# Optimization experiments

Hardware: AMD Instinct MI355X
Metric: run time of the kernel (lower is better)

## Reference

```python
import jax, jax.numpy as jnp
import numpy as np
import math

BL, N, T, C, H = 16, 256, 32, 256, 4
HD = C // H
GEOM_DIM = 12
K_REL = 32
LN_EPS = 1e-5
GEPS = 1e-6
NEG = -1e9


def setup_inputs() -> dict:
    key = jax.random.key(0)
    ks = jax.random.split(key, 24)
    s = 0.02  # weight init scale
    d = {
        "x": jax.random.normal(ks[0], (BL, N, C), jnp.float32),
        "lang_fea": jax.random.normal(ks[1], (BL, T, C), jnp.float32),
        "centers": jax.random.normal(ks[2], (BL, N, 3), jnp.float32),
        "corners": jax.random.normal(ks[3], (BL, N, 8, 3), jnp.float32),
        "obj_mask": jnp.ones((BL, N), dtype=bool),
        # LayerNorm
        "ln_g": jnp.ones((C,), jnp.float32),
        "ln_b": jnp.zeros((C,), jnp.float32),
        # qkv / proj
        "W_qkv": s * jax.random.normal(ks[4], (C, 3 * C), jnp.float32),
        "b_qkv": jnp.zeros((3 * C,), jnp.float32),
        "W_proj": s * jax.random.normal(ks[5], (C, C), jnp.float32),
        "b_proj": jnp.zeros((C,), jnp.float32),
        # geom2bias MLP (12 -> C -> H)
        "Wg1": s * jax.random.normal(ks[6], (GEOM_DIM, C), jnp.float32),
        "bg1": jnp.zeros((C,), jnp.float32),
        "Wg2": s * jax.random.normal(ks[7], (C, H), jnp.float32),
        "bg2": jnp.zeros((H,), jnp.float32),
        # txt2head MLP (C -> C -> H)
        "Wt1": s * jax.random.normal(ks[8], (C, C), jnp.float32),
        "bt1": jnp.zeros((C,), jnp.float32),
        "Wt2": s * jax.random.normal(ks[9], (C, H), jnp.float32),
        "bt2": jnp.zeros((H,), jnp.float32),
        "alpha": jnp.float32(0.05),
    }
    return d


def _build_relation_geom(centers, corners):
    # centers: (BL,N,3), corners: (BL,N,8,3) -> (BL,N,N,12)
    rel_vec = centers[:, None, :, :] - centers[:, :, None, :]  # (BL,N,N,3) j - i
    dist = jnp.linalg.norm(rel_vec, axis=-1, keepdims=True)
    horiz_dist = jnp.linalg.norm(rel_vec[..., :2], axis=-1, keepdims=True)
    delta_z = rel_vec[..., 2:3]
    cos_elev = delta_z / (dist + GEPS)
    sizes = corners.max(axis=2) - corners.min(axis=2)  # (BL,N,3)
    size_i = sizes[:, :, None, :]
    size_j = sizes[:, None, :, :]
    size_diff = size_j - size_i
    size_ratio = size_j / (size_i + GEPS)
    return jnp.concatenate([rel_vec, dist, horiz_dist, cos_elev, size_diff, size_ratio], axis=-1)


def _knn_mask(centers, k):
    # (BL,N,N) bool: each row i keeps its k nearest columns j (incl. self)
    diff = centers[:, :, None, :] - centers[:, None, :, :]
    dist = jnp.linalg.norm(diff, axis=-1)  # (BL,N,N)
    _, idx = jax.lax.top_k(-dist, k)  # smallest-k indices, (BL,N,k)
    return jnp.any(jax.nn.one_hot(idx, dist.shape[-1], dtype=bool), axis=-2)


def reference(x, lang_fea, centers, corners, obj_mask, ln_g, ln_b,
              W_qkv, b_qkv, W_proj, b_proj, Wg1, bg1, Wg2, bg2,
              Wt1, bt1, Wt2, bt2, alpha):
    # geometric pairwise bias: (BL,N,N,12) -> MLP -> (BL,H,N,N)
    geom = _build_relation_geom(centers, corners)
    bias = jax.nn.gelu(geom @ Wg1 + bg1, approximate=False) @ Wg2 + bg2
    bias = jnp.transpose(bias, (0, 3, 1, 2))  # (BL,H,N,N)

    # language-conditioned head gate: (BL,H,1,1)
    sent = lang_fea.mean(axis=1)  # (BL,C)
    head_w = jax.nn.sigmoid(jax.nn.gelu(sent @ Wt1 + bt1, approximate=False) @ Wt2 + bt2)
    head_w = head_w[:, :, None, None]

    warm = 1.0  # epoch=None -> no warmup scaling

    knn_mask = _knn_mask(centers, K_REL)
    pair = obj_mask[:, :, None] & obj_mask[:, None, :]
    attn_mask = knn_mask & pair  # (BL,N,N)

    residual = x
    # LayerNorm
    mu = x.mean(axis=-1, keepdims=True)
    var = x.var(axis=-1, keepdims=True)
    xn = (x - mu) * jax.lax.rsqrt(var + LN_EPS) * ln_g + ln_b

    qkv = (xn @ W_qkv + b_qkv).reshape(BL, N, 3, H, HD)
    q = jnp.transpose(qkv[:, :, 0], (0, 2, 1, 3))  # (BL,H,N,HD)
    k = jnp.transpose(qkv[:, :, 1], (0, 2, 1, 3))
    v = jnp.transpose(qkv[:, :, 2], (0, 2, 1, 3))

    logits = jnp.einsum("bhid,bhjd->bhij", q, k) / math.sqrt(HD)
    bias_eff = warm * alpha * head_w * bias
    logits = logits + bias_eff
    logits = jnp.where(attn_mask[:, None, :, :], logits, NEG)

    attn = jax.nn.softmax(logits, axis=-1)  # dropout is identity at eval
    out = jnp.einsum("bhij,bhjd->bhid", attn, v)
    out = jnp.transpose(out, (0, 2, 1, 3)).reshape(BL, N, C)
    out = out @ W_proj + b_proj
    x_out = residual + out
    return (x_out, jax.lax.stop_gradient(attn), jax.lax.stop_gradient(bias_eff))
```

## Files before the change

### kernel.cpp

```cpp
#include <hip/hip_runtime.h>
#include <math.h>

#define BLn 16
#define Nn 256
#define Tn 32
#define Cn 256
#define Hn 4
#define HDn 64
#define KREL 32

typedef float f32x4 __attribute__((ext_vector_type(4)));
typedef __bf16 bf16x8 __attribute__((ext_vector_type(8)));

#define MFMA16(a, b, c) __builtin_amdgcn_mfma_f32_16x16x32_bf16(a, b, c, 0, 0, 0)

union frag_u {
    bf16x8 v;
    uint2 u[2];
};

__device__ __forceinline__ float gelu_exact(float x) {
    return 0.5f * x * (1.0f + erff(x * 0.70710678118654752440f));
}

__device__ __forceinline__ float gelu_sig(float x) {
    float e = __builtin_amdgcn_exp2f(-2.4554669f * x);
    return x * __builtin_amdgcn_rcpf(1.0f + e);
}

__global__ void __launch_bounds__(256) k_prep(
    const float* __restrict__ x, const float* __restrict__ ln_g, const float* __restrict__ ln_b,
    __bf16* __restrict__ xnb, const float* __restrict__ centers, const int* __restrict__ obj,
    unsigned char* __restrict__ knn, const float* __restrict__ corners,
    float* __restrict__ sizes, const float* __restrict__ lang, const float* __restrict__ Wt1,
    const float* __restrict__ bt1, const float* __restrict__ Wt2, const float* __restrict__ bt2,
    float* __restrict__ headw, const float* __restrict__ W_qkv, __bf16* __restrict__ wqT,
    const float* __restrict__ W_proj, __bf16* __restrict__ wpT) {
    __shared__ float4 d4[64];
    __shared__ float sm1[Nn];
    __shared__ float ss[4], qq[4];
    __shared__ float T[64][65];
    float* sm0 = (float*)d4;
    int blk = blockIdx.x;
    int tid = threadIdx.x;

    if (blk < 4096) {
        int row = blk;
        int c = tid;
        float v = x[(size_t)row * Cn + c];
        float s = v, q = v * v;
        for (int m = 32; m > 0; m >>= 1) {
            s += __shfl_xor(s, m, 64);
            q += __shfl_xor(q, m, 64);
        }
        int w = c >> 6, l = c & 63;
        if (l == 0) { ss[w] = s; qq[w] = q; }
        __syncthreads();
        s = ss[0] + ss[1] + ss[2] + ss[3];
        q = qq[0] + qq[1] + qq[2] + qq[3];
        float mu = s * (1.0f / Cn);
        float var = q * (1.0f / Cn) - mu * mu;
        float r = rsqrtf(var + 1e-5f);
        xnb[(size_t)row * Cn + c] = (__bf16)((v - mu) * r * ln_g[c] + ln_b[c]);
    } else if (blk < 8192) {
        int bi = blk - 4096;
        int b = bi >> 8, i = bi & 255;
        int j = tid;
        float cx = centers[(b * Nn + i) * 3 + 0];
        float cy = centers[(b * Nn + i) * 3 + 1];
        float cz = centers[(b * Nn + i) * 3 + 2];
        float dx = centers[(b * Nn + j) * 3 + 0] - cx;
        float dy = centers[(b * Nn + j) * 3 + 1] - cy;
        float dz = centers[(b * Nn + j) * 3 + 2] - cz;
        float dd = sqrtf(dx * dx + dy * dy + dz * dz);
        sm0[j] = dd;
        __syncthreads();
        int rank = 0;
        for (int t4 = 0; t4 < 64; t4++) {
            float4 o = d4[t4];
            int t = t4 * 4;
            rank += (o.x < dd) || (o.x == dd && t + 0 < j);
            rank += (o.y < dd) || (o.y == dd && t + 1 < j);
            rank += (o.z < dd) || (o.z == dd && t + 2 < j);
            rank += (o.w < dd) || (o.w == dd && t + 3 < j);
        }
        bool m = (rank < KREL);
        m = m && (obj[b * Nn + i] != 0) && (obj[b * Nn + j] != 0);
        knn[(size_t)bi * Nn + j] = m ? 1 : 0;
    } else if (blk < 8208) {
        int b = blk - 8192, n = tid;
        const float* p = corners + (size_t)((b * Nn + n) * 8) * 3;
        float mn[3] = {1e30f, 1e30f, 1e30f}, mx[3] = {-1e30f, -1e30f, -1e30f};
        for (int v = 0; v < 8; v++)
            for (int d = 0; d < 3; d++) {
                float t = p[v * 3 + d];
                mn[d] = fminf(mn[d], t);
                mx[d] = fmaxf(mx[d], t);
            }
        for (int d = 0; d < 3; d++) sizes[(b * Nn + n) * 3 + d] = mx[d] - mn[d];
    } else if (blk < 8224) {
        int b = blk - 8208, c = tid;
        float s = 0.0f;
        for (int t = 0; t < Tn; t++) s += lang[((size_t)b * Tn + t) * Cn + c];
        sm0[c] = s * (1.0f / Tn);
        __syncthreads();
        float acc = bt1[c];
        for (int i = 0; i < Cn; i++) acc += sm0[i] * Wt1[i * Cn + c];
        sm1[c] = gelu_exact(acc);
        __syncthreads();
        if (c < Hn) {
            float a = bt2[c];
            for (int i = 0; i < Cn; i++) a += sm1[i] * Wt2[i * Hn + c];
            headw[b * Hn + c] = 1.0f / (1.0f + expf(-a));
        }
    } else if (blk < 8272) {
        int t = blk - 8224;
        int kt = t & 3, ot = t >> 2;
        for (int itr = 0; itr < 16; itr++) {
            int idx = itr * 256 + tid;
            int r = idx >> 6, c = idx & 63;
            T[r][c] = W_qkv[(size_t)(kt * 64 + r) * 768 + ot * 64 + c];
        }
        __syncthreads();
        for (int itr = 0; itr < 16; itr++) {
            int idx = itr * 256 + tid;
            int r = idx >> 6, c = idx & 63;
            wqT[(size_t)(ot * 64 + r) * 256 + kt * 64 + c] = (__bf16)T[c][r];
        }
    } else {
        int t = blk - 8272;
        int kt = t & 3, ot = t >> 2;
        for (int itr = 0; itr < 16; itr++) {
            int idx = itr * 256 + tid;
            int r = idx >> 6, c = idx & 63;
            T[r][c] = W_proj[(size_t)(kt * 64 + r) * 256 + ot * 64 + c];
        }
        __syncthreads();
        for (int itr = 0; itr < 16; itr++) {
            int idx = itr * 256 + tid;
            int r = idx >> 6, c = idx & 63;
            wpT[(size_t)(ot * 64 + r) * 256 + kt * 64 + c] = (__bf16)T[c][r];
        }
    }
}

__global__ void __launch_bounds__(256, 5) k_heavy(
    const float* __restrict__ centers, const float* __restrict__ sizes,
    const float* __restrict__ Wg1, const float* __restrict__ bg1,
    const float* __restrict__ Wg2, const float* __restrict__ bg2,
    const float* __restrict__ headw, const float* __restrict__ alphap,
    float* __restrict__ bias_eff, const __bf16* __restrict__ xnb,
    const __bf16* __restrict__ wqT, const float* __restrict__ bqkv,
    __bf16* __restrict__ qkvb) {
    __shared__ __bf16 fT[Nn][16];
    __shared__ __bf16 W1T[257][20];
    __shared__ __bf16 W2T[4][260];
    __shared__ __bf16 gbuf[4][32][40];

    int blk = blockIdx.x;
    int tid = threadIdx.x;

    if (blk >= 4096) {
        int t = blk - 4096;
        int ib = t & 63, y = t >> 6;
        int w = tid >> 6, l = tid & 63, lr = l & 15, lg = l >> 4;
        const __bf16* arow = xnb + (size_t)(ib * 64 + w * 16 + lr) * Cn;

        f32x4 acc[4];
#pragma unroll
        for (int ot = 0; ot < 4; ot++) acc[ot] = (f32x4){0.f, 0.f, 0.f, 0.f};
#pragma unroll
        for (int kc = 0; kc < 8; kc++) {
            bf16x8 af = *(const bf16x8*)(arow + kc * 32 + lg * 8);
#pragma unroll
            for (int ot = 0; ot < 4; ot++) {
                bf16x8 bfr = *(const bf16x8*)(wqT + (size_t)(y * 64 + ot * 16 + lr) * Cn +
                                              kc * 32 + lg * 8);
                acc[ot] = MFMA16(af, bfr, acc[ot]);
            }
        }
        int seg = y >> 2, h = y & 3;
        __bf16* segp = qkvb + (size_t)seg * 1048576;
#pragma unroll
        for (int ot = 0; ot < 4; ot++) {
            float bo = bqkv[y * 64 + ot * 16 + lr];
#pragma unroll
            for (int r = 0; r < 4; r++) {
                int ig = ib * 64 + w * 16 + lg * 4 + r;
                int b = ig >> 8, n = ig & 255;
                segp[(((size_t)(b * Hn + h)) * Nn + n) * HDn + ot * 16 + lr] =
                    (__bf16)(acc[ot][r] + bo);
            }
        }
        return;
    }

    int b = blk >> 8, i = blk & 255;

    {
        int c = tid;
        __bf16 t1[20];
#pragma unroll
        for (int k = 0; k < 12; k++) t1[k] = (__bf16)Wg1[k * Cn + c];
        t1[12] = (__bf16)bg1[c];
#pragma unroll
        for (int k = 13; k < 20; k++) t1[k] = (__bf16)0.f;
#pragma unroll
        for (int q = 0; q < 5; q++) *(uint2*)&W1T[c][q * 4] = *(uint2*)&t1[q * 4];
#pragma unroll
        for (int h = 0; h < Hn; h++) W2T[h][c] = (__bf16)Wg2[c * Hn + h];
    }
    {
        int j = tid;
        float ci0 = centers[(b * Nn + i) * 3 + 0];
        float ci1 = centers[(b * Nn + i) * 3 + 1];
        float ci2 = centers[(b * Nn + i) * 3 + 2];
        float si0 = sizes[(b * Nn + i) * 3 + 0];
        float si1 = sizes[(b * Nn + i) * 3 + 1];
        float si2 = sizes[(b * Nn + i) * 3 + 2];
        float cj0 = centers[(b * Nn + j) * 3 + 0];
        float cj1 = centers[(b * Nn + j) * 3 + 1];
        float cj2 = centers[(b * Nn + j) * 3 + 2];
        float sj0 = sizes[(b * Nn + j) * 3 + 0];
        float sj1 = sizes[(b * Nn + j) * 3 + 1];
        float sj2 = sizes[(b * Nn + j) * 3 + 2];
        float rx = cj0 - ci0, ry = cj1 - ci1, rz = cj2 - ci2;
        float h2 = rx * rx + ry * ry;
        float dist = sqrtf(h2 + rz * rz);
        float horiz = sqrtf(h2);
        float f[16];
        f[0] = rx; f[1] = ry; f[2] = rz;
        f[3] = dist; f[4] = horiz;
        f[5] = rz / (dist + 1e-6f);
        f[6] = sj0 - si0; f[7] = sj1 - si1; f[8] = sj2 - si2;
        f[9] = sj0 / (si0 + 1e-6f);
        f[10] = sj1 / (si1 + 1e-6f);
        f[11] = sj2 / (si2 + 1e-6f);
        f[12] = 1.0f;
        __bf16 tf[16];
#pragma unroll
        for (int k = 0; k < 13; k++) tf[k] = (__bf16)f[k];
#pragma unroll
        for (int k = 13; k < 16; k++) tf[k] = (__bf16)0.f;
        *(bf16x8*)&fT[j][0] = *(bf16x8*)&tf[0];
        *(bf16x8*)&fT[j][8] = *(bf16x8*)&tf[8];
    }
    __syncthreads();

    int w = tid >> 6, l = tid & 63;
    int lr = l & 15, lg = l >> 4;
    int jw = w * 64;
    int lgc = (lg < 2) ? lg : 1;
    bool hk = (lg < 2);
    int lrc = (lr < 4) ? lr : 3;
    bool hr = (lr < 4);

    bf16x8 zf;
#pragma unroll
    for (int e = 0; e < 8; e++) zf[e] = (__bf16)0.f;
    f32x4 zero4 = {0.f, 0.f, 0.f, 0.f};

    bf16x8 bf_[4];
#pragma unroll
    for (int jt = 0; jt < 4; jt++) {
        bf16x8 v = *(const bf16x8*)&fT[jw + jt * 16 + lr][lgc * 8];
        bf_[jt] = hk ? v : zf;
    }

    f32x4 pacc[4];
#pragma unroll
    for (int jt = 0; jt < 4; jt++) pacc[jt] = zero4;

    for (int cc = 0; cc < 8; cc++) {
        int cbase = cc * 32;
        bf16x8 aw[2];
#pragma unroll
        for (int ct = 0; ct < 2; ct++) {
            frag_u fu;
            const __bf16* p = &W1T[cbase + ct * 16 + lr][lgc * 8];
            fu.u[0] = *(const uint2*)p;
            fu.u[1] = *(const uint2*)(p + 4);
            aw[ct] = hk ? fu.v : zf;
        }
        frag_u f2;
        {
            const __bf16* p2 = &W2T[lrc][cbase + lg * 8];
            f2.u[0] = *(const uint2*)p2;
            f2.u[1] = *(const uint2*)(p2 + 4);
        }
        bf16x8 b2 = hr ? f2.v : zf;

#pragma unroll
        for (int jp = 0; jp < 2; jp++) {
#pragma unroll
            for (int j2 = 0; j2 < 2; j2++) {
                int jt = jp * 2 + j2;
                f32x4 a0 = MFMA16(aw[0], bf_[jt], zero4);
                f32x4 a1 = MFMA16(aw[1], bf_[jt], zero4);
                __bf16 g0[4], g1[4];
#pragma unroll
                for (int r = 0; r < 4; r++) {
                    g0[r] = (__bf16)gelu_sig(a0[r]);
                    g1[r] = (__bf16)gelu_sig(a1[r]);
                }
                *(uint2*)&gbuf[w][j2 * 16 + lr][lg * 4] = *(uint2*)g0;
                *(uint2*)&gbuf[w][j2 * 16 + lr][16 + lg * 4] = *(uint2*)g1;
            }
#pragma unroll
            for (int j2 = 0; j2 < 2; j2++) {
                int jt = jp * 2 + j2;
                bf16x8 a2 = *(const bf16x8*)&gbuf[w][j2 * 16 + lr][lg * 8];
                pacc[jt] = MFMA16(a2, b2, pacc[jt]);
            }
        }
    }

    float alpha = alphap[0];
    if (hr) {
        float hw_ = headw[b * Hn + lr];
        float bg = bg2[lr];
        float* dst = bias_eff + (((size_t)(b * Hn + lr)) * Nn + i) * Nn;
#pragma unroll
        for (int jt = 0; jt < 4; jt++) {
            f32x4 o4;
#pragma unroll
            for (int r = 0; r < 4; r++) o4[r] = alpha * hw_ * (pacc[jt][r] + bg);
            *(f32x4*)&dst[jw + jt * 16 + lg * 4] = o4;
        }
    }
}

__global__ void __launch_bounds__(256) k_attn(const __bf16* __restrict__ qkvb,
                                              const float* __restrict__ bias_eff,
                                              const unsigned char* __restrict__ knn,
                                              float* __restrict__ attn_out,
                                              __bf16* __restrict__ houtb) {
    __shared__ __bf16 Vt[64][264];
    __shared__ __bf16 Plds[4][16][136];
    int blk = blockIdx.x;
    int bh = blk >> 2, it = blk & 3;
    int b = bh >> 2, h = bh & 3;
    int tid = threadIdx.x;

    const __bf16* vbase = qkvb + 2 * 1048576 + (size_t)bh * (Nn * HDn);
    {
        int j = tid;
#pragma unroll
        for (int c8 = 0; c8 < 8; c8++) {
            bf16x8 v8 = *(const bf16x8*)(vbase + (size_t)j * HDn + c8 * 8);
#pragma unroll
            for (int e = 0; e < 8; e++) Vt[c8 * 8 + e][j] = v8[e];
        }
    }
    __syncthreads();

    int w = tid >> 6, l = tid & 63;
    int lr = l & 15, lg = l >> 4;
    int i_glob = it * 64 + w * 16 + lr;

    const __bf16* qrow = qkvb + (size_t)bh * (Nn * HDn) + (size_t)i_glob * HDn;
    bf16x8 qf0 = *(const bf16x8*)(qrow + lg * 8);
    bf16x8 qf1 = *(const bf16x8*)(qrow + 32 + lg * 8);

    const __bf16* kbase = qkvb + 1048576 + (size_t)bh * (Nn * HDn);
    f32x4 s[16];
#pragma unroll
    for (int jt = 0; jt < 16; jt++) {
        const __bf16* krow = kbase + (size_t)(jt * 16 + lr) * HDn;
        bf16x8 ka = *(const bf16x8*)(krow + lg * 8);
        bf16x8 kb = *(const bf16x8*)(krow + 32 + lg * 8);
        f32x4 acc = (f32x4){0.f, 0.f, 0.f, 0.f};
        acc = MFMA16(ka, qf0, acc);
        acc = MFMA16(kb, qf1, acc);
        s[jt] = acc;
    }

    const float* brow = bias_eff + ((size_t)bh * Nn + i_glob) * Nn;
    const unsigned int* mrow = (const unsigned int*)(knn + ((size_t)(b * Nn + i_glob)) * Nn);
    float mx = -1e30f;
#pragma unroll
    for (int jt = 0; jt < 16; jt++) {
        f32x4 bi = *(const f32x4*)(brow + jt * 16 + lg * 4);
        unsigned int mk = mrow[jt * 4 + lg];
#pragma unroll
        for (int r = 0; r < 4; r++) {
            float v = fmaf(s[jt][r], 0.125f, bi[r]);
            v = ((mk >> (8 * r)) & 0xff) ? v : -1e9f;
            s[jt][r] = v;
            mx = fmaxf(mx, v);
        }
    }
    mx = fmaxf(mx, __shfl_xor(mx, 16, 64));
    mx = fmaxf(mx, __shfl_xor(mx, 32, 64));
    float sum = 0.0f;
#pragma unroll
    for (int jt = 0; jt < 16; jt++)
#pragma unroll
        for (int r = 0; r < 4; r++) {
            float e = __builtin_amdgcn_exp2f((s[jt][r] - mx) * 1.44269504f);
            s[jt][r] = e;
            sum += e;
        }
    sum += __shfl_xor(sum, 16, 64);
    sum += __shfl_xor(sum, 32, 64);
    float inv = 1.0f / sum;

    float* arow = attn_out + ((size_t)bh * Nn + i_glob) * Nn;
#pragma unroll
    for (int jt = 0; jt < 16; jt++) {
        f32x4 o4;
#pragma unroll
        for (int r = 0; r < 4; r++) {
            float a = s[jt][r] * inv;
            s[jt][r] = a;
            o4[r] = a;
        }
        *(f32x4*)(arow + jt * 16 + lg * 4) = o4;
    }

    f32x4 o[4];
#pragma unroll
    for (int dt = 0; dt < 4; dt++) o[dt] = (f32x4){0.f, 0.f, 0.f, 0.f};
    for (int half = 0; half < 2; half++) {
#pragma unroll
        for (int jr = 0; jr < 8; jr++) {
            int jt = half * 8 + jr;
            __bf16 pb[4];
#pragma unroll
            for (int r = 0; r < 4; r++) pb[r] = (__bf16)s[jt][r];
            *(uint2*)&Plds[w][lr][jr * 16 + lg * 4] = *(uint2*)pb;
        }
#pragma unroll
        for (int kk = 0; kk < 4; kk++) {
            bf16x8 pfrag = *(const bf16x8*)&Plds[w][lr][kk * 32 + lg * 8];
#pragma unroll
            for (int dt = 0; dt < 4; dt++) {
                bf16x8 vfrag = *(const bf16x8*)&Vt[dt * 16 + lr][half * 128 + kk * 32 + lg * 8];
                o[dt] = MFMA16(vfrag, pfrag, o[dt]);
            }
        }
    }

    __bf16* hrow = houtb + ((size_t)(b * Nn + i_glob)) * Cn + h * HDn;
#pragma unroll
    for (int dt = 0; dt < 4; dt++) {
        __bf16 hb[4];
#pragma unroll
        for (int r = 0; r < 4; r++) hb[r] = (__bf16)o[dt][r];
        *(uint2*)(hrow + dt * 16 + lg * 4) = *(uint2*)hb;
    }
}

__global__ void __launch_bounds__(256) k_proj(const __bf16* __restrict__ houtb,
                                              const __bf16* __restrict__ wpT,
                                              const float* __restrict__ bp,
                                              const float* __restrict__ x,
                                              float* __restrict__ xout) {
    int ib = blockIdx.x, y = blockIdx.y;
    int tid = threadIdx.x;
    int w = tid >> 6, l = tid & 63, lr = l & 15, lg = l >> 4;
    const __bf16* arow = houtb + (size_t)(ib * 64 + w * 16 + lr) * Cn;

    f32x4 acc[4];
#pragma unroll
    for (int ot = 0; ot < 4; ot++) acc[ot] = (f32x4){0.f, 0.f, 0.f, 0.f};
#pragma unroll
    for (int kc = 0; kc < 8; kc++) {
        bf16x8 af = *(const bf16x8*)(arow + kc * 32 + lg * 8);
#pragma unroll
        for (int ot = 0; ot < 4; ot++) {
            bf16x8 bfr = *(const bf16x8*)(wpT + (size_t)(y * 64 + ot * 16 + lr) * Cn +
                                          kc * 32 + lg * 8);
            acc[ot] = MFMA16(af, bfr, acc[ot]);
        }
    }
#pragma unroll
    for (int ot = 0; ot < 4; ot++) {
        int o = y * 64 + ot * 16 + lr;
        float bo = bp[o];
#pragma unroll
        for (int r = 0; r < 4; r++) {
            int ig = ib * 64 + w * 16 + lg * 4 + r;
            size_t idx = (size_t)ig * Cn + o;
            xout[idx] = x[idx] + bo + acc[ot][r];
        }
    }
}

extern "C" void kernel_launch(void* const* d_in, const int* in_sizes, int n_in,
                              void* d_out, int out_size, void* d_ws, size_t ws_size,
                              hipStream_t stream) {
    const float* x       = (const float*)d_in[0];
    const float* lang    = (const float*)d_in[1];
    const float* centers = (const float*)d_in[2];
    const float* corners = (const float*)d_in[3];
    const int*   obj     = (const int*)d_in[4];
    const float* ln_g    = (const float*)d_in[5];
    const float* ln_b    = (const float*)d_in[6];
    const float* W_qkv   = (const float*)d_in[7];
    const float* b_qkv   = (const float*)d_in[8];
    const float* W_proj  = (const float*)d_in[9];
    const float* b_proj  = (const float*)d_in[10];
    const float* Wg1     = (const float*)d_in[11];
    const float* bg1     = (const float*)d_in[12];
    const float* Wg2     = (const float*)d_in[13];
    const float* bg2     = (const float*)d_in[14];
    const float* Wt1     = (const float*)d_in[15];
    const float* bt1     = (const float*)d_in[16];
    const float* Wt2     = (const float*)d_in[17];
    const float* bt2     = (const float*)d_in[18];
    const float* alpha   = (const float*)d_in[19];

    float* out = (float*)d_out;
    float* xout     = out;
    float* attn     = out + 1048576;
    float* bias_eff = out + 5242880;

    __bf16* xnb   = (__bf16*)d_ws;
    __bf16* qkvb  = xnb + 1048576;
    __bf16* houtb = qkvb + 3145728;
    __bf16* wqT   = houtb + 1048576;
    __bf16* wpT   = wqT + 196608;
    float*  sizes = (float*)(wpT + 65536);
    float*  headw = sizes + 12288;
    unsigned char* knn = (unsigned char*)(headw + 64);

    k_prep<<<8288, 256, 0, stream>>>(x, ln_g, ln_b, xnb, centers, obj, knn, corners, sizes,
                                     lang, Wt1, bt1, Wt2, bt2, headw, W_qkv, wqT, W_proj, wpT);
    k_heavy<<<4864, 256, 0, stream>>>(centers, sizes, Wg1, bg1, Wg2, bg2, headw, alpha,
                                      bias_eff, xnb, wqT, b_qkv, qkvb);
    k_attn<<<256, 256, 0, stream>>>(qkvb, bias_eff, knn, attn, houtb);
    k_proj<<<dim3(64, 4), 256, 0, stream>>>(houtb, wpT, b_proj, x, xout);
}
```

Measured before the change: 144.8 us.

## Use fp16 16x16x16 MFMA with packed polynomial GELU in geometry-bias MLP

Replaces the bf16 32-K MFMA geom-bias MLP with fp16 16x16x16 MFMAs. The GELU output stays in registers and feeds the second MFMA directly, which removes the LDS round trip through gbuf. GELU becomes a packed fp16 clamped polynomial instead of exp2/rcp, and wasted padded K lanes are no longer computed. Risks include fp16 accuracy of the approximate GELU and lower occupancy from the launch bound changing from 5 to 4.

Result: faster. 122.0 us (-15.7%).

```diff
diff --git a/kernel.cpp b/kernel.cpp
--- a/kernel.cpp
+++ b/kernel.cpp
@@ -11,21 +11,35 @@
 
 typedef float f32x4 __attribute__((ext_vector_type(4)));
 typedef __bf16 bf16x8 __attribute__((ext_vector_type(8)));
+typedef _Float16 f16x4 __attribute__((ext_vector_type(4)));
+typedef _Float16 f16x2 __attribute__((ext_vector_type(2)));
 
 #define MFMA16(a, b, c) __builtin_amdgcn_mfma_f32_16x16x32_bf16(a, b, c, 0, 0, 0)
-
-union frag_u {
-    bf16x8 v;
-    uint2 u[2];
-};
+#define MFMA16H(a, b, c) __builtin_amdgcn_mfma_f32_16x16x16f16(a, b, c, 0, 0, 0)
 
 __device__ __forceinline__ float gelu_exact(float x) {
     return 0.5f * x * (1.0f + erff(x * 0.70710678118654752440f));
 }
 
-__device__ __forceinline__ float gelu_sig(float x) {
-    float e = __builtin_amdgcn_exp2f(-2.4554669f * x);
-    return x * __builtin_amdgcn_rcpf(1.0f + e);
+__device__ __forceinline__ f16x2 gelu_pk(f16x2 x) {
+    const f16x2 P4 = {(_Float16)4.0f, (_Float16)4.0f};
+    const f16x2 M4 = {(_Float16)-4.0f, (_Float16)-4.0f};
+    const f16x2 C0 = {(_Float16)0.833076f, (_Float16)0.833076f};
+    const f16x2 C1 = {(_Float16)-0.139388f, (_Float16)-0.139388f};
+    const f16x2 C2 = {(_Float16)0.013040f, (_Float16)0.013040f};
+    const f16x2 C3 = {(_Float16)-0.000413f, (_Float16)-0.000413f};
+    const f16x2 HF = {(_Float16)0.5f, (_Float16)0.5f};
+    const f16x2 ONE = {(_Float16)1.0f, (_Float16)1.0f};
+    const f16x2 ZERO = {(_Float16)0.0f, (_Float16)0.0f};
+    f16x2 xc = __builtin_elementwise_min(__builtin_elementwise_max(x, M4), P4);
+    f16x2 v = xc * xc;
+    f16x2 w = C3 * v + C2;
+    w = w * v + C1;
+    w = w * v + C0;
+    f16x2 t = w * xc;
+    f16x2 s = t * HF + HF;
+    s = __builtin_elementwise_min(__builtin_elementwise_max(s, ZERO), ONE);
+    return x * s;
 }
 
 __global__ void __launch_bounds__(256) k_prep(
@@ -144,7 +158,7 @@
     }
 }
 
-__global__ void __launch_bounds__(256, 5) k_heavy(
+__global__ void __launch_bounds__(256, 4) k_heavy(
     const float* __restrict__ centers, const float* __restrict__ sizes,
     const float* __restrict__ Wg1, const float* __restrict__ bg1,
     const float* __restrict__ Wg2, const float* __restrict__ bg2,
@@ -152,10 +166,9 @@
     float* __restrict__ bias_eff, const __bf16* __restrict__ xnb,
     const __bf16* __restrict__ wqT, const float* __restrict__ bqkv,
     __bf16* __restrict__ qkvb) {
-    __shared__ __bf16 fT[Nn][16];
-    __shared__ __bf16 W1T[257][20];
-    __shared__ __bf16 W2T[4][260];
-    __shared__ __bf16 gbuf[4][32][40];
+    __shared__ __align__(16) _Float16 fT[Nn][20];
+    __shared__ __align__(16) _Float16 W1T[Cn][20];
+    __shared__ __align__(16) _Float16 W2T[16][264];
 
     int blk = blockIdx.x;
     int tid = threadIdx.x;
@@ -199,16 +212,17 @@
 
     {
         int c = tid;
-        __bf16 t1[20];
-#pragma unroll
-        for (int k = 0; k < 12; k++) t1[k] = (__bf16)Wg1[k * Cn + c];
-        t1[12] = (__bf16)bg1[c];
-#pragma unroll
-        for (int k = 13; k < 20; k++) t1[k] = (__bf16)0.f;
+        _Float16 t1[20];
+#pragma unroll
+        for (int k = 0; k < 12; k++) t1[k] = (_Float16)Wg1[k * Cn + c];
+        t1[12] = (_Float16)bg1[c];
+#pragma unroll
+        for (int k = 13; k < 20; k++) t1[k] = (_Float16)0.f;
 #pragma unroll
         for (int q = 0; q < 5; q++) *(uint2*)&W1T[c][q * 4] = *(uint2*)&t1[q * 4];
 #pragma unroll
-        for (int h = 0; h < Hn; h++) W2T[h][c] = (__bf16)Wg2[c * Hn + h];
+        for (int h = 0; h < 16; h++)
+            W2T[h][c] = (h < Hn) ? (_Float16)Wg2[c * Hn + h] : (_Float16)0.f;
     }
     {
         int j = tid;
@@ -237,86 +251,50 @@
         f[10] = sj1 / (si1 + 1e-6f);
         f[11] = sj2 / (si2 + 1e-6f);
         f[12] = 1.0f;
-        __bf16 tf[16];
-#pragma unroll
-        for (int k = 0; k < 13; k++) tf[k] = (__bf16)f[k];
-#pragma unroll
-        for (int k = 13; k < 16; k++) tf[k] = (__bf16)0.f;
-        *(bf16x8*)&fT[j][0] = *(bf16x8*)&tf[0];
-        *(bf16x8*)&fT[j][8] = *(bf16x8*)&tf[8];
+        _Float16 tf[20];
+#pragma unroll
+        for (int k = 0; k < 13; k++) tf[k] = (_Float16)f[k];
+#pragma unroll
+        for (int k = 13; k < 20; k++) tf[k] = (_Float16)0.f;
+#pragma unroll
+        for (int q = 0; q < 5; q++) *(uint2*)&fT[j][q * 4] = *(uint2*)&tf[q * 4];
     }
     __syncthreads();
 
     int w = tid >> 6, l = tid & 63;
     int lr = l & 15, lg = l >> 4;
     int jw = w * 64;
-    int lgc = (lg < 2) ? lg : 1;
-    bool hk = (lg < 2);
-    int lrc = (lr < 4) ? lr : 3;
-    bool hr = (lr < 4);
-
-    bf16x8 zf;
-#pragma unroll
-    for (int e = 0; e < 8; e++) zf[e] = (__bf16)0.f;
+
     f32x4 zero4 = {0.f, 0.f, 0.f, 0.f};
 
-    bf16x8 bf_[4];
-#pragma unroll
-    for (int jt = 0; jt < 4; jt++) {
-        bf16x8 v = *(const bf16x8*)&fT[jw + jt * 16 + lr][lgc * 8];
-        bf_[jt] = hk ? v : zf;
-    }
+    f16x4 bf_[4];
+#pragma unroll
+    for (int jt = 0; jt < 4; jt++) bf_[jt] = *(const f16x4*)&fT[jw + jt * 16 + lr][lg * 4];
 
     f32x4 pacc[4];
 #pragma unroll
     for (int jt = 0; jt < 4; jt++) pacc[jt] = zero4;
 
-    for (int cc = 0; cc < 8; cc++) {
-        int cbase = cc * 32;
-        bf16x8 aw[2];
-#pragma unroll
-        for (int ct = 0; ct < 2; ct++) {
-            frag_u fu;
-            const __bf16* p = &W1T[cbase + ct * 16 + lr][lgc * 8];
-            fu.u[0] = *(const uint2*)p;
-            fu.u[1] = *(const uint2*)(p + 4);
-            aw[ct] = hk ? fu.v : zf;
-        }
-        frag_u f2;
-        {
-            const __bf16* p2 = &W2T[lrc][cbase + lg * 8];
-            f2.u[0] = *(const uint2*)p2;
-            f2.u[1] = *(const uint2*)(p2 + 4);
-        }
-        bf16x8 b2 = hr ? f2.v : zf;
-
-#pragma unroll
-        for (int jp = 0; jp < 2; jp++) {
-#pragma unroll
-            for (int j2 = 0; j2 < 2; j2++) {
-                int jt = jp * 2 + j2;
-                f32x4 a0 = MFMA16(aw[0], bf_[jt], zero4);
-                f32x4 a1 = MFMA16(aw[1], bf_[jt], zero4);
-                __bf16 g0[4], g1[4];
-#pragma unroll
-                for (int r = 0; r < 4; r++) {
-                    g0[r] = (__bf16)gelu_sig(a0[r]);
-                    g1[r] = (__bf16)gelu_sig(a1[r]);
-                }
-                *(uint2*)&gbuf[w][j2 * 16 + lr][lg * 4] = *(uint2*)g0;
-                *(uint2*)&gbuf[w][j2 * 16 + lr][16 + lg * 4] = *(uint2*)g1;
-            }
-#pragma unroll
-            for (int j2 = 0; j2 < 2; j2++) {
-                int jt = jp * 2 + j2;
-                bf16x8 a2 = *(const bf16x8*)&gbuf[w][j2 * 16 + lr][lg * 8];
-                pacc[jt] = MFMA16(a2, b2, pacc[jt]);
-            }
+#pragma unroll 2
+    for (int cw = 0; cw < 16; cw++) {
+        int cbase = cw * 16;
+        f16x4 aw = *(const f16x4*)&W1T[cbase + lr][lg * 4];
+        f16x4 b2 = *(const f16x4*)&W2T[lr][cbase + lg * 4];
+#pragma unroll
+        for (int jt = 0; jt < 4; jt++) {
+            f32x4 acc = MFMA16H(aw, bf_[jt], zero4);
+            f16x2 h01 = __builtin_bit_cast(f16x2, __builtin_amdgcn_cvt_pkrtz(acc[0], acc[1]));
+            f16x2 h23 = __builtin_bit_cast(f16x2, __builtin_amdgcn_cvt_pkrtz(acc[2], acc[3]));
+            h01 = gelu_pk(h01);
+            h23 = gelu_pk(h23);
+            f16x4 ga;
+            ga[0] = h01[0]; ga[1] = h01[1]; ga[2] = h23[0]; ga[3] = h23[1];
+            pacc[jt] = MFMA16H(ga, b2, pacc[jt]);
         }
     }
 
     float alpha = alphap[0];
-    if (hr) {
+    if (lr < Hn) {
         float hw_ = headw[b * Hn + lr];
         float bg = bg2[lr];
         float* dst = bias_eff + (((size_t)(b * Hn + lr)) * Nn + i) * Nn;
```
